# Kernel tuning notes

Measured on AMD Instinct MI355X. Metric: run time of the kernel, lower is better.

## Reference

```python
import jax, jax.numpy as jnp
import numpy as np

B, N, C = 8, 2048, 320
CQ = C // 5  # query/key channel dim = 64


def setup_inputs() -> dict:
    key = jax.random.key(0)
    ks = jax.random.split(key, 8)
    s = 0.05
    return {
        "x": jax.random.normal(ks[0], (B, N, C), dtype=jnp.float32),
        "Wq": jax.random.normal(ks[1], (CQ, C), dtype=jnp.float32) * s,
        "bq": jax.random.normal(ks[2], (CQ,), dtype=jnp.float32) * s,
        "Wk": jax.random.normal(ks[3], (CQ, C), dtype=jnp.float32) * s,
        "bk": jax.random.normal(ks[4], (CQ,), dtype=jnp.float32) * s,
        "Wv": jax.random.normal(ks[5], (C, C), dtype=jnp.float32) * s,
        "bv": jax.random.normal(ks[6], (C,), dtype=jnp.float32) * s,
        "gamma": jnp.zeros((1,), dtype=jnp.float32) + 0.5,
    }


def reference(x, Wq, bq, Wk, bk, Wv, bv, gamma):
    # x: (B, N, C). torch module permutes to (B, C, N) and uses 1x1 Conv1d,
    # which is a per-position linear over channels.
    q = jnp.einsum("bnc,qc->bnq", x, Wq) + bq          # (B, N, CQ) proj_query
    k = jnp.einsum("bnc,qc->bqn", x, Wk) + bk[:, None]  # (B, CQ, N) proj_key
    energy = jnp.einsum("bnq,bqm->bnm", q, k)           # (B, N, N)
    attention = jax.nn.softmax(energy, axis=-1)          # softmax over last dim
    v = jnp.einsum("bnc,dc->bdn", x, Wv) + bv[:, None]  # (B, C, N) proj_value
    # torch: out = bmm(V (B,C,N), A (B,N,N)) -> out[b,c,n] = sum_k V[b,c,k]*A[b,k,n]
    out = jnp.einsum("bck,bkn->bcn", v, attention)       # (B, C, N)
    out = gamma[0] * out + jnp.swapaxes(x, 1, 2)         # residual on (B, C, N)
    return jnp.swapaxes(out, 1, 2)                       # (B, N, C)
```

## Files before the change

### kernel.cpp

```cpp
#include <hip/hip_runtime.h>
#include <hip/hip_bf16.h>

#define BB 8
#define NN 2048
#define CC 320
#define CQ 64
#define LOG2E 1.4426950408889634f

typedef __attribute__((ext_vector_type(8)))  short bf16x8;
typedef __attribute__((ext_vector_type(4)))  float f32x4;
typedef __attribute__((ext_vector_type(16))) float f32x16;
typedef __attribute__((ext_vector_type(4)))  unsigned short us4;
typedef __attribute__((ext_vector_type(8)))  unsigned short us8;
typedef __attribute__((ext_vector_type(4)))  unsigned int u32x4;
typedef unsigned short u16;


static __device__ __forceinline__ u16 f2b(float f) {
  unsigned u = __builtin_bit_cast(unsigned, f);
  unsigned r = (u + 0x7FFFu + ((u >> 16) & 1u)) >> 16;
  return (u16)r;
}
static __device__ __forceinline__ float b2f(u16 s) {
  unsigned u = ((unsigned)s) << 16;
  return __builtin_bit_cast(float, u);
}

static __device__ __forceinline__ f32x16 zero16() {
  f32x16 v = {0,0,0,0, 0,0,0,0, 0,0,0,0, 0,0,0,0};
  return v;
}
static __device__ __forceinline__ f32x4 zero4() {
  f32x4 v = {0,0,0,0};
  return v;
}

static __device__ __forceinline__ void gll16(const void* g, void* l) {
  __builtin_amdgcn_global_load_lds(
      (const __attribute__((address_space(1))) unsigned int*)g,
      (__attribute__((address_space(3))) unsigned int*)l, 16, 0, 0);
}

static __device__ __forceinline__ bf16x8 cvt8(float4 a, float4 b) {
  unsigned p0, p1, p2, p3;
  asm("v_cvt_pk_bf16_f32 %0, %1, %2" : "=v"(p0) : "v"(a.x), "v"(a.y));
  asm("v_cvt_pk_bf16_f32 %0, %1, %2" : "=v"(p1) : "v"(a.z), "v"(a.w));
  asm("v_cvt_pk_bf16_f32 %0, %1, %2" : "=v"(p2) : "v"(b.x), "v"(b.y));
  asm("v_cvt_pk_bf16_f32 %0, %1, %2" : "=v"(p3) : "v"(b.z), "v"(b.w));
  u32x4 w = {p0, p1, p2, p3};
  return __builtin_bit_cast(bf16x8, w);
}

__global__ __launch_bounds__(256) void cvt_x_blk(const float* __restrict__ x,
                                                 u16* __restrict__ X3) {
  __shared__ float xs[32][324];
  const int t = threadIdx.x;
  const int b = blockIdx.x;
  const size_t srcb = (size_t)b * 32 * CC;
#pragma unroll
  for (int i = 0; i < 10; ++i) {
    const int lidx = i * 256 + t;
    const int m = lidx / 80;
    const int kq = lidx - m * 80;
    float4 v = *(const float4*)(x + srcb + (size_t)m * CC + kq * 4);
    *(float4*)&xs[m][kq * 4] = v;
  }
  __syncthreads();
  u16* dst0 = X3 + (size_t)b * 10240;
#pragma unroll
  for (int i = 0; i < 5; ++i) {
    const int u = i * 256 + t;
    const int kk8 = u >> 5, ml = u & 31;
    float4 a = *(const float4*)&xs[ml][kk8 * 8];
    float4 c = *(const float4*)&xs[ml][kk8 * 8 + 4];
    bf16x8 o = cvt8(a, c);
    *(bf16x8*)(dst0 + (size_t)u * 8) = o;
  }
}

__global__ __launch_bounds__(256) void cvt_w_blk(const float* __restrict__ Wq,
                                                 const float* __restrict__ Wk,
                                                 const float* __restrict__ Wv,
                                                 u16* __restrict__ W3) {
  __shared__ float xs[32][324];
  const int t = threadIdx.x;
  const int b = blockIdx.x;
#pragma unroll
  for (int i = 0; i < 10; ++i) {
    const int lidx = i * 256 + t;
    const int m = lidx / 80;
    const int kq = lidx - m * 80;
    const int row = b * 32 + m;
    const float* src = (row < 64) ? (Wq + (size_t)row * CC)
                     : (row < 128) ? (Wk + (size_t)(row - 64) * CC)
                                   : (Wv + (size_t)(row - 128) * CC);
    float4 v = *(const float4*)(src + kq * 4);
    *(float4*)&xs[m][kq * 4] = v;
  }
  __syncthreads();
  u16* dst0 = W3 + (size_t)b * 10240;
#pragma unroll
  for (int i = 0; i < 5; ++i) {
    const int u = i * 256 + t;
    const int kk8 = u >> 5, ml = u & 31;
    float4 a = *(const float4*)&xs[ml][kk8 * 8];
    float4 c = *(const float4*)&xs[ml][kk8 * 8 + 4];
    bf16x8 o = cvt8(a, c);
    *(bf16x8*)(dst0 + (size_t)u * 8) = o;
  }
}

__global__ __launch_bounds__(256) void gemm_qkv(
    const u16* __restrict__ X3, const u16* __restrict__ W3,
    const float* __restrict__ bq, const float* __restrict__ bk,
    const float* __restrict__ bv,
    u16* __restrict__ Qb, u16* __restrict__ Kb, u16* __restrict__ Vt) {
  const int tid = threadIdx.x;
  const int lane = tid & 63, wid = tid >> 6;
  const int r = lane & 31, h = lane >> 5;
  const int bid = blockIdx.x;
  const int xcd = bid & 7;
  const int slot = bid >> 3;
  const int colt = slot % 7;
  const int yG = slot / 7;
  const int ytile = yG * 8 + xcd;
  const int m0 = ytile * 128 + wid * 32;
  const int col0 = colt * 64;
  const int mt = m0 >> 5;

  const u16* abase  = X3 + (size_t)mt * 10240 + (size_t)h * 256 + r * 8;
  const u16* b0base = W3 + (size_t)(colt * 2) * 10240 + (size_t)h * 256 + r * 8;
  const u16* b1base = b0base + 10240;

  f32x16 acc0 = zero16(), acc1 = zero16();
  bf16x8 a   = *(const bf16x8*)(abase);
  bf16x8 b0v = *(const bf16x8*)(b0base);
  bf16x8 b1v = *(const bf16x8*)(b1base);
#pragma unroll 1
  for (int ks = 0; ks < 20; ++ks) {
    bf16x8 na, nb0, nb1;
    if (ks < 19) {
      na  = *(const bf16x8*)(abase  + (ks + 1) * 512);
      nb0 = *(const bf16x8*)(b0base + (ks + 1) * 512);
      nb1 = *(const bf16x8*)(b1base + (ks + 1) * 512);
    }
    acc0 = __builtin_amdgcn_mfma_f32_32x32x16_bf16(a, b0v, acc0, 0, 0, 0);
    acc1 = __builtin_amdgcn_mfma_f32_32x32x16_bf16(a, b1v, acc1, 0, 0, 0);
    a = na; b0v = nb0; b1v = nb1;
  }

  const int bb = m0 >> 11;
  const int mloc = m0 & 2047;

#pragma unroll
  for (int nt = 0; nt < 2; ++nt) {
    const int col = col0 + nt * 32 + r;
    const f32x16 A = nt ? acc1 : acc0;
    if (col0 >= 128) {
      const int c = col - 128;
      const float bias = bv[c];
      u16* vdst = Vt + (((size_t)(bb * 256 + (mloc >> 3)) * 320 + c) * 8) + 4 * h;
#pragma unroll
      for (int g = 0; g < 4; ++g) {
        us4 o;
#pragma unroll
        for (int e = 0; e < 4; ++e) o[e] = f2b(A[g * 4 + e] + bias);
        *(us4*)(vdst + (size_t)g * 2560) = o;
      }
    } else if (col0 >= 64) {
      const float bias = bk[col - 64];
#pragma unroll
      for (int reg = 0; reg < 16; ++reg) {
        const int row = m0 + (reg & 3) + 8 * (reg >> 2) + 4 * h;
        Kb[(size_t)row * CQ + (col - 64)] = f2b(A[reg] + bias);
      }
    } else {
      const float bias = bq[col];
      const int kt = mloc >> 5;
      u16* qdst = Qb + (((size_t)(bb * 64 + kt) * 8 + (col >> 3)) * 32) * 8 + (col & 7);
#pragma unroll
      for (int reg = 0; reg < 16; ++reg) {
        const int kl = (reg & 3) + 8 * (reg >> 2) + 4 * h;
        qdst[kl * 8] = f2b((A[reg] + bias) * LOG2E);
      }
    }
  }
}

__global__ __launch_bounds__(512) void row_stats(
    const u16* __restrict__ Qb, const u16* __restrict__ Kb,
    u16* __restrict__ Vt) {
  __shared__ float Sp[8][64];
  __shared__ float sInv[64];
  const int tid = threadIdx.x;
  const int lane = tid & 63, wid = tid >> 6;
  const int rl = lane & 15, hq = lane >> 4;
  const int bid = blockIdx.x;
  const int batch = bid & 7;
  const int kloc64 = (bid >> 3) * 64;

  bf16x8 af[4][2];
#pragma unroll
  for (int mt = 0; mt < 4; ++mt) {
    const int k_loc = kloc64 + mt * 16 + rl;
    const int kt = k_loc >> 5, kl = k_loc & 31;
#pragma unroll
    for (int qs = 0; qs < 2; ++qs)
      af[mt][qs] = *(const bf16x8*)(Qb +
          (((size_t)(batch * 64 + kt) * 8 + qs * 4 + hq) * 32 + kl) * 8);
  }

  float S[4][4];
#pragma unroll
  for (int mt = 0; mt < 4; ++mt)
#pragma unroll
    for (int rr = 0; rr < 4; ++rr) S[mt][rr] = 0.f;

  const int mstart = batch * NN + wid * 256;
  const u16* kr = Kb + (size_t)(mstart + rl) * CQ + hq * 8;
  bf16x8 c0 = *(const bf16x8*)(kr);
  bf16x8 c1 = *(const bf16x8*)(kr + 32);
#pragma unroll 1
  for (int ms = 0; ms < 16; ++ms) {
    bf16x8 n0, n1;
    if (ms < 15) {
      n0 = *(const bf16x8*)(kr + 16 * CQ);
      n1 = *(const bf16x8*)(kr + 16 * CQ + 32);
    }
#pragma unroll
    for (int mt = 0; mt < 4; ++mt) {
      f32x4 e = zero4();
      e = __builtin_amdgcn_mfma_f32_16x16x32_bf16(af[mt][0], c0, e, 0, 0, 0);
      e = __builtin_amdgcn_mfma_f32_16x16x32_bf16(af[mt][1], c1, e, 0, 0, 0);
#pragma unroll
      for (int rr = 0; rr < 4; ++rr) S[mt][rr] += __builtin_amdgcn_exp2f(e[rr]);
    }
    c0 = n0; c1 = n1; kr += 16 * CQ;
  }

#pragma unroll
  for (int d = 1; d < 16; d <<= 1)
#pragma unroll
    for (int mt = 0; mt < 4; ++mt)
#pragma unroll
      for (int rr = 0; rr < 4; ++rr) S[mt][rr] += __shfl_xor(S[mt][rr], d, 64);

  if (rl == 0) {
#pragma unroll
    for (int mt = 0; mt < 4; ++mt)
#pragma unroll
      for (int rr = 0; rr < 4; ++rr) Sp[wid][mt * 16 + hq * 4 + rr] = S[mt][rr];
  }
  __syncthreads();
  if (tid < 64) {
    float s = 0.f;
#pragma unroll
    for (int p = 0; p < 8; ++p) s += Sp[p][tid];
    sInv[tid] = 1.0f / s;
  }
  __syncthreads();

  const int kt8b = kloc64 >> 3;
#pragma unroll 1
  for (int i = 0; i < 10; ++i) {
    const int chunk = i * 512 + tid;
    const int kt8l = chunk / 640;
    const int rem = chunk - kt8l * 640;
    const int c = rem >> 1;
    const int h2 = rem & 1;
    u16* p = Vt + (((size_t)(batch * 256 + kt8b + kt8l) * 320 + c) * 8) + h2 * 4;
    us4 v = *(const us4*)p;
    us4 o;
#pragma unroll
    for (int e2 = 0; e2 < 4; ++e2) o[e2] = f2b(b2f(v[e2]) * sInv[kt8l * 8 + h2 * 4 + e2]);
    *(us4*)p = o;
  }
}

__global__ __launch_bounds__(256, 2) void attn(
    const u16* __restrict__ Qb, const u16* __restrict__ Kb,
    const u16* __restrict__ Vt, const float* __restrict__ x,
    const float* __restrict__ gamma, float* __restrict__ out) {
  __shared__ __align__(16) char LDSRAW[40960];
  const int tid = threadIdx.x;
  const int lane = tid & 63, wid = tid >> 6;
  const int wn = wid >> 1;
  const int kh = wid & 1;
  const int r = lane & 31, h = lane >> 5;
  const int bid = blockIdx.x;
  const int b = bid & 7;
  const int rest = bid >> 3;
  const int ch = rest & 1;
  const int n0 = (rest >> 1) * 64;

  bf16x8 kf[4];
  {
    const u16* krow = Kb + (size_t)(b * NN + n0 + wn * 32 + r) * CQ + h * 8;
#pragma unroll
    for (int qs = 0; qs < 4; ++qs) kf[qs] = *(const bf16x8*)(krow + qs * 16);
  }

  f32x16 acc[5];
#pragma unroll
  for (int j = 0; j < 5; ++j) acc[j] = zero16();

  const u16* qb3 = Qb + ((size_t)(b * 64 + kh * 32) * 8) * 256 + (size_t)r * 8;

#define STAGE(TN, BUF) {                                                       \
    _Pragma("unroll")                                                          \
    for (int i_ = 0; i_ < 5; ++i_) {                                           \
      const int c_ = wid * 5 + i_;                                             \
      const int khc_ = c_ / 10;                                                \
      const int rem_ = c_ % 10;                                                \
      char* dst_ = LDSRAW + (BUF) * 20480 + khc_ * 10240 + rem_ * 1024;        \
      const int off_ = rem_ * 512 + lane * 8;                                  \
      const int row_ = off_ / 1280;                                            \
      const int win_ = off_ - row_ * 1280;                                     \
      const u16* src_ = Vt +                                                   \
          ((size_t)(b * 256 + khc_ * 128 + (TN) * 4 + row_) * 320              \
           + ch * 160) * 8 + win_;                                             \
      gll16(src_, dst_);                                                       \
    }                                                                          \
  }

#define LQ(QN, TN) {                                                           \
    _Pragma("unroll")                                                          \
    for (int qs = 0; qs < 4; ++qs)                                             \
      QN[qs] = *(const bf16x8*)(qb3 + ((size_t)(TN) * 8 + qs * 2 + h) * 256);  \
  }

#define COMPUTE(T, BUF, QF, QN, TNX) {                                         \
    LQ(QN, TNX)                                                                \
    const char* base_ = LDSRAW + (BUF) * 20480 + kh * 10240;                   \
    f32x16 e = zero16();                                                       \
    _Pragma("unroll")                                                          \
    for (int qs = 0; qs < 4; ++qs)                                             \
      e = __builtin_amdgcn_mfma_f32_32x32x16_bf16(QF[qs], kf[qs], e, 0, 0, 0); \
    bf16x8 vf[5][2];                                                           \
    _Pragma("unroll")                                                          \
    for (int j = 0; j < 5; ++j)                                                \
      _Pragma("unroll")                                                        \
      for (int ks = 0; ks < 2; ++ks)                                           \
        vf[j][ks] = *(const bf16x8*)(base_ + (ks * 2 + h) * 2560               \
                                     + (j * 32 + r) * 16);                     \
    unsigned pk0, pk1, pk2, pk3, pk4, pk5, pk6, pk7;                           \
    { float l0 = __builtin_amdgcn_exp2f(e[0]),  h0 = __builtin_amdgcn_exp2f(e[1]);  \
      float l1 = __builtin_amdgcn_exp2f(e[2]),  h1 = __builtin_amdgcn_exp2f(e[3]);  \
      float l2 = __builtin_amdgcn_exp2f(e[4]),  h2 = __builtin_amdgcn_exp2f(e[5]);  \
      float l3 = __builtin_amdgcn_exp2f(e[6]),  h3 = __builtin_amdgcn_exp2f(e[7]);  \
      float l4 = __builtin_amdgcn_exp2f(e[8]),  h4 = __builtin_amdgcn_exp2f(e[9]);  \
      float l5 = __builtin_amdgcn_exp2f(e[10]), h5 = __builtin_amdgcn_exp2f(e[11]); \
      float l6 = __builtin_amdgcn_exp2f(e[12]), h6 = __builtin_amdgcn_exp2f(e[13]); \
      float l7 = __builtin_amdgcn_exp2f(e[14]), h7 = __builtin_amdgcn_exp2f(e[15]); \
      asm("v_cvt_pk_bf16_f32 %0, %1, %2" : "=v"(pk0) : "v"(l0), "v"(h0));      \
      asm("v_cvt_pk_bf16_f32 %0, %1, %2" : "=v"(pk1) : "v"(l1), "v"(h1));      \
      asm("v_cvt_pk_bf16_f32 %0, %1, %2" : "=v"(pk2) : "v"(l2), "v"(h2));      \
      asm("v_cvt_pk_bf16_f32 %0, %1, %2" : "=v"(pk3) : "v"(l3), "v"(h3));      \
      asm("v_cvt_pk_bf16_f32 %0, %1, %2" : "=v"(pk4) : "v"(l4), "v"(h4));      \
      asm("v_cvt_pk_bf16_f32 %0, %1, %2" : "=v"(pk5) : "v"(l5), "v"(h5));      \
      asm("v_cvt_pk_bf16_f32 %0, %1, %2" : "=v"(pk6) : "v"(l6), "v"(h6));      \
      asm("v_cvt_pk_bf16_f32 %0, %1, %2" : "=v"(pk7) : "v"(l7), "v"(h7)); }    \
    asm("v_permlane32_swap_b32 %0, %1" : "+v"(pk0), "+v"(pk2));                \
    asm("v_permlane32_swap_b32 %0, %1" : "+v"(pk1), "+v"(pk3));                \
    asm("v_permlane32_swap_b32 %0, %1" : "+v"(pk4), "+v"(pk6));                \
    asm("v_permlane32_swap_b32 %0, %1" : "+v"(pk5), "+v"(pk7));                \
    u32x4 w0_ = {pk0, pk1, pk2, pk3};                                          \
    u32x4 w1_ = {pk4, pk5, pk6, pk7};                                          \
    bf16x8 pa0 = __builtin_bit_cast(bf16x8, w0_);                              \
    bf16x8 pa1 = __builtin_bit_cast(bf16x8, w1_);                              \
    _Pragma("unroll")                                                          \
    for (int j = 0; j < 5; ++j) {                                              \
      acc[j] = __builtin_amdgcn_mfma_f32_32x32x16_bf16(pa0, vf[j][0], acc[j], 0, 0, 0); \
      acc[j] = __builtin_amdgcn_mfma_f32_32x32x16_bf16(pa1, vf[j][1], acc[j], 0, 0, 0); \
    }                                                                          \
  }

  bf16x8 qfA[4], qfB[4];

  STAGE(0, 0);
  LQ(qfA, 0)
  __syncthreads();
#pragma unroll 1
  for (int t = 0; t < 32; t += 2) {
    STAGE(t + 1, 1);
    COMPUTE(t, 0, qfA, qfB, t + 1);
    __syncthreads();
    if (t + 2 < 32) STAGE(t + 2, 0);
    COMPUTE(t + 1, 1, qfB, qfA, (t + 2) & 31);
    __syncthreads();
  }
#undef STAGE
#undef LQ
#undef COMPUTE

  float* red = (float*)LDSRAW;
  if (kh == 1) {
#pragma unroll
    for (int reg = 0; reg < 16; ++reg) {
      const int nl = (reg & 3) + 8 * (reg >> 2) + 4 * h;
#pragma unroll
      for (int j = 0; j < 5; ++j)
        red[wn * 5120 + nl * 160 + j * 32 + r] = acc[j][reg];
    }
  }
  __syncthreads();
  if (kh == 0) {
    const float g = gamma[0];
#pragma unroll
    for (int reg = 0; reg < 16; ++reg) {
      const int nl = (reg & 3) + 8 * (reg >> 2) + 4 * h;
      const size_t rowb = ((size_t)(b * NN) + n0 + wn * 32 + nl) * CC + ch * 160 + r;
#pragma unroll
      for (int j = 0; j < 5; ++j) {
        const size_t idx = rowb + (size_t)(j * 32);
        const float s = acc[j][reg] + red[wn * 5120 + nl * 160 + j * 32 + r];
        out[idx] = g * s + x[idx];
      }
    }
  }
}

extern "C" void kernel_launch(void* const* d_in, const int* in_sizes, int n_in,
                              void* d_out, int out_size, void* d_ws, size_t ws_size,
                              hipStream_t stream) {
  const float* x     = (const float*)d_in[0];
  const float* Wq    = (const float*)d_in[1];
  const float* bq    = (const float*)d_in[2];
  const float* Wk    = (const float*)d_in[3];
  const float* bk    = (const float*)d_in[4];
  const float* Wv    = (const float*)d_in[5];
  const float* bv    = (const float*)d_in[6];
  const float* gamma = (const float*)d_in[7];
  float* out = (float*)d_out;

  char* w = (char*)d_ws;
  u16* X3 = (u16*)(w);
  u16* W3 = (u16*)(w + 10485760);
  u16* Qb = (u16*)(w + 10772480);
  u16* Kb = (u16*)(w + 12869632);
  u16* Vt = (u16*)(w + 14966784);

  cvt_x_blk<<<512, 256, 0, stream>>>(x, X3);
  cvt_w_blk<<<14, 256, 0, stream>>>(Wq, Wk, Wv, W3);
  gemm_qkv<<<896, 256, 0, stream>>>(X3, W3, bq, bk, bv, Qb, Kb, Vt);
  row_stats<<<256, 512, 0, stream>>>(Qb, Kb, Vt);
  attn<<<512, 256, 0, stream>>>(Qb, Kb, Vt, x, gamma, out);
}
```

Before: 87.11 us.

## Fold softmax normalizer into exp via log2 sum; merge conversion kernels

Instead of rescaling V in place by the inverse row sum in row_stats (a read-modify-write over all of V), row_stats now writes log2 of the softmax denominator to a small buffer. The attn kernel subtracts it inside each exp2 before packing to bf16, loading the needed values alongside the Q fragments. The x and weight conversion kernels are merged into one launch. This removes a full pass over V and one kernel launch. In exchange, attn does extra global loads and subtractions per tile and holds more registers.

```diff
diff --git a/kernel.cpp b/kernel.cpp
--- a/kernel.cpp
+++ b/kernel.cpp
@@ -51,54 +51,36 @@
   return __builtin_bit_cast(bf16x8, w);
 }
 
-__global__ __launch_bounds__(256) void cvt_x_blk(const float* __restrict__ x,
-                                                 u16* __restrict__ X3) {
+__global__ __launch_bounds__(256) void cvt_blk(const float* __restrict__ x,
+                                               const float* __restrict__ Wq,
+                                               const float* __restrict__ Wk,
+                                               const float* __restrict__ Wv,
+                                               u16* __restrict__ X3,
+                                               u16* __restrict__ W3) {
   __shared__ float xs[32][324];
   const int t = threadIdx.x;
-  const int b = blockIdx.x;
-  const size_t srcb = (size_t)b * 32 * CC;
+  const int bid = blockIdx.x;
+  const bool isX = (bid < 512);
+  const int b = isX ? bid : (bid - 512);
 #pragma unroll
   for (int i = 0; i < 10; ++i) {
     const int lidx = i * 256 + t;
     const int m = lidx / 80;
     const int kq = lidx - m * 80;
-    float4 v = *(const float4*)(x + srcb + (size_t)m * CC + kq * 4);
-    *(float4*)&xs[m][kq * 4] = v;
-  }
-  __syncthreads();
-  u16* dst0 = X3 + (size_t)b * 10240;
-#pragma unroll
-  for (int i = 0; i < 5; ++i) {
-    const int u = i * 256 + t;
-    const int kk8 = u >> 5, ml = u & 31;
-    float4 a = *(const float4*)&xs[ml][kk8 * 8];
-    float4 c = *(const float4*)&xs[ml][kk8 * 8 + 4];
-    bf16x8 o = cvt8(a, c);
-    *(bf16x8*)(dst0 + (size_t)u * 8) = o;
-  }
-}
-
-__global__ __launch_bounds__(256) void cvt_w_blk(const float* __restrict__ Wq,
-                                                 const float* __restrict__ Wk,
-                                                 const float* __restrict__ Wv,
-                                                 u16* __restrict__ W3) {
-  __shared__ float xs[32][324];
-  const int t = threadIdx.x;
-  const int b = blockIdx.x;
-#pragma unroll
-  for (int i = 0; i < 10; ++i) {
-    const int lidx = i * 256 + t;
-    const int m = lidx / 80;
-    const int kq = lidx - m * 80;
-    const int row = b * 32 + m;
-    const float* src = (row < 64) ? (Wq + (size_t)row * CC)
-                     : (row < 128) ? (Wk + (size_t)(row - 64) * CC)
-                                   : (Wv + (size_t)(row - 128) * CC);
+    const float* src;
+    if (isX) {
+      src = x + (size_t)(b * 32 + m) * CC;
+    } else {
+      const int row = b * 32 + m;
+      src = (row < 64) ? (Wq + (size_t)row * CC)
+          : (row < 128) ? (Wk + (size_t)(row - 64) * CC)
+                        : (Wv + (size_t)(row - 128) * CC);
+    }
     float4 v = *(const float4*)(src + kq * 4);
     *(float4*)&xs[m][kq * 4] = v;
   }
   __syncthreads();
-  u16* dst0 = W3 + (size_t)b * 10240;
+  u16* dst0 = (isX ? X3 : W3) + (size_t)b * 10240;
 #pragma unroll
   for (int i = 0; i < 5; ++i) {
     const int u = i * 256 + t;
@@ -189,9 +171,8 @@
 
 __global__ __launch_bounds__(512) void row_stats(
     const u16* __restrict__ Qb, const u16* __restrict__ Kb,
-    u16* __restrict__ Vt) {
+    float* __restrict__ Lb) {
   __shared__ float Sp[8][64];
-  __shared__ float sInv[64];
   const int tid = threadIdx.x;
   const int lane = tid & 63, wid = tid >> 6;
   const int rl = lane & 15, hq = lane >> 4;
@@ -256,31 +237,15 @@
     float s = 0.f;
 #pragma unroll
     for (int p = 0; p < 8; ++p) s += Sp[p][tid];
-    sInv[tid] = 1.0f / s;
-  }
-  __syncthreads();
-
-  const int kt8b = kloc64 >> 3;
-#pragma unroll 1
-  for (int i = 0; i < 10; ++i) {
-    const int chunk = i * 512 + tid;
-    const int kt8l = chunk / 640;
-    const int rem = chunk - kt8l * 640;
-    const int c = rem >> 1;
-    const int h2 = rem & 1;
-    u16* p = Vt + (((size_t)(batch * 256 + kt8b + kt8l) * 320 + c) * 8) + h2 * 4;
-    us4 v = *(const us4*)p;
-    us4 o;
-#pragma unroll
-    for (int e2 = 0; e2 < 4; ++e2) o[e2] = f2b(b2f(v[e2]) * sInv[kt8l * 8 + h2 * 4 + e2]);
-    *(us4*)p = o;
+    Lb[batch * NN + kloc64 + tid] = __log2f(s);
   }
 }
 
 __global__ __launch_bounds__(256, 2) void attn(
     const u16* __restrict__ Qb, const u16* __restrict__ Kb,
-    const u16* __restrict__ Vt, const float* __restrict__ x,
-    const float* __restrict__ gamma, float* __restrict__ out) {
+    const u16* __restrict__ Vt, const float* __restrict__ Lb,
+    const float* __restrict__ x, const float* __restrict__ gamma,
+    float* __restrict__ out) {
   __shared__ __align__(16) char LDSRAW[40960];
   const int tid = threadIdx.x;
   const int lane = tid & 63, wid = tid >> 6;
@@ -305,6 +270,7 @@
   for (int j = 0; j < 5; ++j) acc[j] = zero16();
 
   const u16* qb3 = Qb + ((size_t)(b * 64 + kh * 32) * 8) * 256 + (size_t)r * 8;
+  const float* lbase = Lb + b * NN + kh * 1024 + 4 * h;
 
 #define STAGE(TN, BUF) {                                                       \
     _Pragma("unroll")                                                          \
@@ -323,14 +289,17 @@
     }                                                                          \
   }
 
-#define LQ(QN, TN) {                                                           \
+#define LQ(QN, LN, TN) {                                                       \
     _Pragma("unroll")                                                          \
     for (int qs = 0; qs < 4; ++qs)                                             \
       QN[qs] = *(const bf16x8*)(qb3 + ((size_t)(TN) * 8 + qs * 2 + h) * 256);  \
-  }
-
-#define COMPUTE(T, BUF, QF, QN, TNX) {                                         \
-    LQ(QN, TNX)                                                                \
+    _Pragma("unroll")                                                          \
+    for (int g = 0; g < 4; ++g)                                                \
+      LN[g] = *(const float4*)(lbase + (TN) * 32 + g * 8);                     \
+  }
+
+#define COMPUTE(T, BUF, QF, LF, QN, LN, TNX) {                                 \
+    LQ(QN, LN, TNX)                                                            \
     const char* base_ = LDSRAW + (BUF) * 20480 + kh * 10240;                   \
     f32x16 e = zero16();                                                       \
     _Pragma("unroll")                                                          \
@@ -344,14 +313,22 @@
         vf[j][ks] = *(const bf16x8*)(base_ + (ks * 2 + h) * 2560               \
                                      + (j * 32 + r) * 16);                     \
     unsigned pk0, pk1, pk2, pk3, pk4, pk5, pk6, pk7;                           \
-    { float l0 = __builtin_amdgcn_exp2f(e[0]),  h0 = __builtin_amdgcn_exp2f(e[1]);  \
-      float l1 = __builtin_amdgcn_exp2f(e[2]),  h1 = __builtin_amdgcn_exp2f(e[3]);  \
-      float l2 = __builtin_amdgcn_exp2f(e[4]),  h2 = __builtin_amdgcn_exp2f(e[5]);  \
-      float l3 = __builtin_amdgcn_exp2f(e[6]),  h3 = __builtin_amdgcn_exp2f(e[7]);  \
-      float l4 = __builtin_amdgcn_exp2f(e[8]),  h4 = __builtin_amdgcn_exp2f(e[9]);  \
-      float l5 = __builtin_amdgcn_exp2f(e[10]), h5 = __builtin_amdgcn_exp2f(e[11]); \
-      float l6 = __builtin_amdgcn_exp2f(e[12]), h6 = __builtin_amdgcn_exp2f(e[13]); \
-      float l7 = __builtin_amdgcn_exp2f(e[14]), h7 = __builtin_amdgcn_exp2f(e[15]); \
+    { float l0 = __builtin_amdgcn_exp2f(e[0]  - LF[0].x);                      \
+      float h0 = __builtin_amdgcn_exp2f(e[1]  - LF[0].y);                      \
+      float l1 = __builtin_amdgcn_exp2f(e[2]  - LF[0].z);                      \
+      float h1 = __builtin_amdgcn_exp2f(e[3]  - LF[0].w);                      \
+      float l2 = __builtin_amdgcn_exp2f(e[4]  - LF[1].x);                      \
+      float h2 = __builtin_amdgcn_exp2f(e[5]  - LF[1].y);                      \
+      float l3 = __builtin_amdgcn_exp2f(e[6]  - LF[1].z);                      \
+      float h3 = __builtin_amdgcn_exp2f(e[7]  - LF[1].w);                      \
+      float l4 = __builtin_amdgcn_exp2f(e[8]  - LF[2].x);                      \
+      float h4 = __builtin_amdgcn_exp2f(e[9]  - LF[2].y);                      \
+      float l5 = __builtin_amdgcn_exp2f(e[10] - LF[2].z);                      \
+      float h5 = __builtin_amdgcn_exp2f(e[11] - LF[2].w);                      \
+      float l6 = __builtin_amdgcn_exp2f(e[12] - LF[3].x);                      \
+      float h6 = __builtin_amdgcn_exp2f(e[13] - LF[3].y);                      \
+      float l7 = __builtin_amdgcn_exp2f(e[14] - LF[3].z);                      \
+      float h7 = __builtin_amdgcn_exp2f(e[15] - LF[3].w);                      \
       asm("v_cvt_pk_bf16_f32 %0, %1, %2" : "=v"(pk0) : "v"(l0), "v"(h0));      \
       asm("v_cvt_pk_bf16_f32 %0, %1, %2" : "=v"(pk1) : "v"(l1), "v"(h1));      \
       asm("v_cvt_pk_bf16_f32 %0, %1, %2" : "=v"(pk2) : "v"(l2), "v"(h2));      \
@@ -376,17 +353,18 @@
   }
 
   bf16x8 qfA[4], qfB[4];
+  float4 lfA[4], lfB[4];
 
   STAGE(0, 0);
-  LQ(qfA, 0)
+  LQ(qfA, lfA, 0)
   __syncthreads();
 #pragma unroll 1
   for (int t = 0; t < 32; t += 2) {
     STAGE(t + 1, 1);
-    COMPUTE(t, 0, qfA, qfB, t + 1);
+    COMPUTE(t, 0, qfA, lfA, qfB, lfB, t + 1);
     __syncthreads();
     if (t + 2 < 32) STAGE(t + 2, 0);
-    COMPUTE(t + 1, 1, qfB, qfA, (t + 2) & 31);
+    COMPUTE(t + 1, 1, qfB, lfB, qfA, lfA, (t + 2) & 31);
     __syncthreads();
   }
 #undef STAGE
@@ -434,15 +412,15 @@
   float* out = (float*)d_out;
 
   char* w = (char*)d_ws;
-  u16* X3 = (u16*)(w);
-  u16* W3 = (u16*)(w + 10485760);
-  u16* Qb = (u16*)(w + 10772480);
-  u16* Kb = (u16*)(w + 12869632);
-  u16* Vt = (u16*)(w + 14966784);
-
-  cvt_x_blk<<<512, 256, 0, stream>>>(x, X3);
-  cvt_w_blk<<<14, 256, 0, stream>>>(Wq, Wk, Wv, W3);
+  u16* X3   = (u16*)(w);
+  u16* W3   = (u16*)(w + 10485760);
+  u16* Qb   = (u16*)(w + 10772480);
+  u16* Kb   = (u16*)(w + 12869632);
+  u16* Vt   = (u16*)(w + 14966784);
+  float* Lb = (float*)(w + 25452544);
+
+  cvt_blk<<<526, 256, 0, stream>>>(x, Wq, Wk, Wv, X3, W3);
   gemm_qkv<<<896, 256, 0, stream>>>(X3, W3, bq, bk, bv, Qb, Kb, Vt);
-  row_stats<<<256, 512, 0, stream>>>(Qb, Kb, Vt);
-  attn<<<512, 256, 0, stream>>>(Qb, Kb, Vt, x, gamma, out);
-}
+  row_stats<<<256, 512, 0, stream>>>(Qb, Kb, Lb);
+  attn<<<512, 256, 0, stream>>>(Qb, Kb, Vt, Lb, x, gamma, out);
+}
```

New measurement: 83.04 us. 4.7% less time.
